# Kernel optimization log

Measured on AMD Instinct MI355X. Metric: run time of the kernel, lower is better.

Reference implementation:

```python
import jax, jax.numpy as jnp
import numpy as np

N_NODES = 100000
N_EDGES = 1600000
IN_CH = 128
OUT_CH = 128


def setup_inputs() -> dict:
    key = jax.random.key(0)
    k1, k2, k3 = jax.random.split(key, 3)
    x = jax.random.normal(k1, (N_NODES, IN_CH), dtype=jnp.float32)
    edge_index = jax.random.randint(k2, (2, N_EDGES), 0, N_NODES, dtype=jnp.int64)
    # glorot-like init for the linear weight, stored as [in, out]
    W = jax.random.normal(k3, (IN_CH, OUT_CH), dtype=jnp.float32) * (2.0 / (IN_CH + OUT_CH)) ** 0.5
    bias = jnp.zeros((OUT_CH,), dtype=jnp.float32)
    return {"x": x, "edge_index": edge_index, "W": W, "bias": bias}


def reference(x, edge_index, W, bias):
    N = x.shape[0]
    # linear transform (bias-free, matches Linear(in, out, bias=False))
    h = x @ W  # [N, out]

    # add self loops (improved=False -> fill_value = 1.0)
    loop = jnp.arange(N, dtype=edge_index.dtype)
    src = jnp.concatenate([edge_index[0], loop])
    dst = jnp.concatenate([edge_index[1], loop])
    ew = jnp.ones(src.shape[0], dtype=h.dtype)  # edge_weight None -> ones

    # symmetric GCN normalization: deg from dst, norm = d^-1/2[src] * w * d^-1/2[dst]
    deg = jax.ops.segment_sum(ew, dst, num_segments=N)
    deg_inv_sqrt = jnp.where(deg > 0, jax.lax.rsqrt(deg), 0.0)
    w = deg_inv_sqrt[src] * ew * deg_inv_sqrt[dst]

    # spmm aggregation: out[dst] += w * h[src]
    out = jax.ops.segment_sum(h[src] * w[:, None], dst, num_segments=N)
    return out + bias
```

## Files before the change

kernel.cpp:

```cpp
#include <hip/hip_runtime.h>
#include <hip/hip_bf16.h>

constexpr int kNodes = 100000;
constexpr int kEdges = 1600000;
constexpr int kCh    = 128;
constexpr int kCap   = 32;
constexpr int kLOvf  = 256;
constexpr int kBinShift = 7;
constexpr int kBinSize  = 1 << kBinShift;
constexpr int kBins  = (kNodes + kBinSize - 1) >> kBinShift;
constexpr int kABlocks = 128;
constexpr int kChunkCap = 32;
constexpr int kSpillCap = 64;
constexpr int kGemmBlocks = (kNodes + 127) / 128;

typedef __attribute__((ext_vector_type(8))) short short8;
typedef __attribute__((ext_vector_type(4))) float floatx4;
typedef __attribute__((ext_vector_type(4))) int   intx4;
typedef __attribute__((ext_vector_type(2))) float floatx2;


__global__ __launch_bounds__(512) void k_fused(const float* __restrict__ x,
                                               const float* __restrict__ W,
                                               const int* __restrict__ srcArr,
                                               const int* __restrict__ dstArr,
                                               unsigned* __restrict__ segs,
                                               int* __restrict__ segCnt,
                                               int* __restrict__ spillCnt,
                                               int* __restrict__ spillD,
                                               int* __restrict__ spillS,
                                               __hip_bfloat16* __restrict__ hs) {
  if (blockIdx.x < kABlocks) {
    __shared__ int lcnt[kBins];
    __shared__ int lspilln;
    for (int i = threadIdx.x; i < kBins; i += 512) lcnt[i] = 0;
    if (threadIdx.x == 0) lspilln = 0;
    __syncthreads();
    const intx4* d4 = (const intx4*)dstArr;
    const intx4* s4 = (const intx4*)srcArr;
    unsigned* myseg = segs + (long)blockIdx.x * kBins * kChunkCap;
    for (int i = blockIdx.x * 512 + (int)threadIdx.x; i < kEdges / 4; i += kABlocks * 512) {
      intx4 dv = __builtin_nontemporal_load(d4 + i);
      intx4 sv = __builtin_nontemporal_load(s4 + i);
      #pragma unroll
      for (int k = 0; k < 4; k++) {
        int d = dv[k], s = sv[k];
        int bin = d >> kBinShift;
        int pos = atomicAdd(&lcnt[bin], 1);
        if (pos < kChunkCap) {
          myseg[(bin << 5) + pos] = ((unsigned)(d & (kBinSize - 1)) << 17) | (unsigned)s;
        } else {
          int o = atomicAdd(&lspilln, 1);
          if (o < kSpillCap) {
            spillD[blockIdx.x * kSpillCap + o] = d;
            spillS[blockIdx.x * kSpillCap + o] = s;
          }
        }
      }
    }
    __syncthreads();
    for (int i = threadIdx.x; i < kBins; i += 512) {
      int c = lcnt[i];
      segCnt[blockIdx.x * kBins + i] = c < kChunkCap ? c : kChunkCap;
    }
    if (threadIdx.x == 0) {
      int n = lspilln;
      spillCnt[blockIdx.x] = n < kSpillCap ? n : kSpillCap;
    }
    return;
  }

  if (blockIdx.x == kABlocks && threadIdx.x < 64) {
    ((float*)(hs + (long)kNodes * kCh))[threadIdx.x] = 0.0f;
  }

  __shared__ short8 Bf[2048];
  for (int e = threadIdx.x; e < 2048; e += 512) {
    int lane = e & 63, c = (e >> 6) & 3, tt = e >> 8;
    int quad = lane >> 4, mcol = lane & 15;
    short8 v;
    #pragma unroll
    for (int j = 0; j < 8; j++) {
      __hip_bfloat16 h = __float2bfloat16(W[(c * 32 + quad * 8 + j) * kCh + tt * 16 + mcol]);
      v[j] = *(short*)&h;
    }
    Bf[e] = v;
  }
  __syncthreads();

  int wave = threadIdx.x >> 6;
  int lane = threadIdx.x & 63;
  int quad = lane >> 4;
  int mcol = lane & 15;
  int gb = blockIdx.x - kABlocks;
  long rowBase = ((long)gb * 8 + wave) * 16;
  if (rowBase >= kNodes) return;

  long arow = rowBase + mcol;
  if (arow >= kNodes) arow = kNodes - 1;
  const float* xp = x + arow * kCh;
  short8 afrag[4];
  #pragma unroll
  for (int c = 0; c < 4; c++) {
    const floatx4* p = (const floatx4*)(xp + c * 32 + quad * 8);
    floatx4 v0 = __builtin_nontemporal_load(p);
    floatx4 v1 = __builtin_nontemporal_load(p + 1);
    #pragma unroll
    for (int j = 0; j < 4; j++) {
      __hip_bfloat16 h0 = __float2bfloat16(v0[j]);
      __hip_bfloat16 h1 = __float2bfloat16(v1[j]);
      afrag[c][j]     = *(short*)&h0;
      afrag[c][j + 4] = *(short*)&h1;
    }
  }

  #pragma unroll
  for (int t = 0; t < 8; t++) {
    floatx4 acc = {0.f, 0.f, 0.f, 0.f};
    #pragma unroll
    for (int c = 0; c < 4; c++) {
      short8 b = Bf[(t * 4 + c) * 64 + lane];
      acc = __builtin_amdgcn_mfma_f32_16x16x32_bf16(afrag[c], b, acc, 0, 0, 0);
    }
    #pragma unroll
    for (int i = 0; i < 4; i++) {
      long r = rowBase + quad * 4 + i;
      if (r < kNodes) {
        __hip_bfloat16 h = __float2bfloat16(acc[i]);
        __builtin_nontemporal_store(*(short*)&h, (short*)hs + r * kCh + t * 16 + mcol);
      }
    }
  }
}


__global__ __launch_bounds__(256) void k_dinv(const unsigned* __restrict__ segs,
                                              const int* __restrict__ segCnt,
                                              const int* __restrict__ spillCnt,
                                              const int* __restrict__ spillD,
                                              float* __restrict__ dinv) {
  __shared__ int lsn[kABlocks];
  __shared__ int lsp[kABlocks];
  __shared__ int hist[kBinSize];
  int bin = blockIdx.x;
  for (int i = threadIdx.x; i < kABlocks; i += 256) {
    lsn[i] = segCnt[i * kBins + bin];
    lsp[i] = spillCnt[i];
  }
  for (int i = threadIdx.x; i < kBinSize; i += 256) hist[i] = 0;
  __syncthreads();

  for (int slot = threadIdx.x; slot < kABlocks * kChunkCap; slot += 256) {
    int blk = slot >> 5, pos = slot & 31;
    if (pos < lsn[blk]) {
      unsigned e = segs[((long)blk * kBins + bin) * kChunkCap + pos];
      atomicAdd(&hist[e >> 17], 1);
    }
  }
  for (int i = threadIdx.x; i < kABlocks * kSpillCap; i += 256) {
    int blk = i >> 6, o = i & 63;
    if (o < lsp[blk]) {
      int d = spillD[blk * kSpillCap + o];
      if ((d >> kBinShift) == bin) atomicAdd(&hist[d & (kBinSize - 1)], 1);
    }
  }
  __syncthreads();
  int base = bin << kBinShift;
  for (int i = threadIdx.x; i < kBinSize; i += 256) {
    int node = base + i;
    if (node < kNodes) dinv[node] = rsqrtf((float)(hist[i] + 1));
  }
  if (bin == 0 && threadIdx.x == 0) dinv[kNodes] = 0.0f;
}


__global__ __launch_bounds__(512) void k_agg(const unsigned* __restrict__ segs,
                                             const int* __restrict__ segCnt,
                                             const int* __restrict__ spillCnt,
                                             const int* __restrict__ spillD,
                                             const int* __restrict__ spillS,
                                             const float* __restrict__ dinv,
                                             const __hip_bfloat16* __restrict__ hs,
                                             const float* __restrict__ bias,
                                             float* __restrict__ out) {
  __shared__ int lsn[kABlocks];
  __shared__ int lsp[kABlocks];
  __shared__ int lcnt[kBinSize];
  __shared__ __align__(16) int lbkt[kBinSize][kCap];
  __shared__ unsigned lovf[kLOvf];
  __shared__ int lovfn;

  int bin  = blockIdx.x;
  int base = bin << kBinShift;

  for (int i = threadIdx.x; i < kABlocks; i += 512) {
    lsn[i] = segCnt[i * kBins + bin];
    lsp[i] = spillCnt[i];
  }
  for (int i = threadIdx.x; i < kBinSize; i += 512) lcnt[i] = 0;
  if (threadIdx.x == 0) lovfn = 0;
  __syncthreads();

  for (int slot = threadIdx.x; slot < kABlocks * kChunkCap; slot += 512) {
    int blk = slot >> 5, pos = slot & 31;
    if (pos < lsn[blk]) {
      unsigned e = segs[((long)blk * kBins + bin) * kChunkCap + pos];
      int r = (int)(e >> 17);
      int p = atomicAdd(&lcnt[r], 1);
      if (p < kCap) lbkt[r][p] = (int)(e & 0x1ffff);
      else { int o = atomicAdd(&lovfn, 1); if (o < kLOvf) lovf[o] = ((unsigned)r << 17) | (e & 0x1ffff); }
    }
  }
  for (int i = threadIdx.x; i < kABlocks * kSpillCap; i += 512) {
    int blk = i >> 6, o = i & 63;
    if (o < lsp[blk]) {
      int d = spillD[blk * kSpillCap + o];
      if ((d >> kBinShift) == bin) {
        int r = d & (kBinSize - 1);
        int s = spillS[blk * kSpillCap + o];
        int p = atomicAdd(&lcnt[r], 1);
        if (p < kCap) lbkt[r][p] = s;
        else { int o2 = atomicAdd(&lovfn, 1); if (o2 < kLOvf) lovf[o2] = ((unsigned)r << 17) | (unsigned)s; }
      }
    }
  }
  __syncthreads();

  for (int r = threadIdx.x; r < kBinSize; r += 512) {
    int c = lcnt[r]; if (c > kCap) c = kCap;
    int cP = (c + 7) & ~7; if (cP > kCap) cP = kCap;
    for (int p = c; p < cP; p++) lbkt[r][p] = kNodes;
  }
  __syncthreads();

  int wave = threadIdx.x >> 6;
  int lane = threadIdx.x & 63;
  const __hip_bfloat162* hbase = (const __hip_bfloat162*)hs;
  int novf = lovfn; if (novf > kLOvf) novf = kLOvf;
  float2 bsv = ((const float2*)bias)[lane];

  #define ISSUE(S, DV, V, B)                                                     \
    _Pragma("unroll")                                                            \
    for (int u = 0; u < 8; u++) S[u] = lbkt[r][(B) * 8 + u];                     \
    _Pragma("unroll")                                                            \
    for (int u = 0; u < 8; u++) { DV[u] = dinv[S[u]];                            \
      V[u] = hbase[(long)S[u] * (kCh / 2) + lane]; }

  #define CONSUME(DV, V)                                                         \
    _Pragma("unroll")                                                            \
    for (int u = 0; u < 8; u++) { float2 f = __bfloat1622float2(V[u]);           \
      acc0 = fmaf(DV[u], f.x, acc0); acc1 = fmaf(DV[u], f.y, acc1); }

  for (int t = 0; t < 16; t++) {
    int r = wave * 16 + t;
    int node = base + r;
    if (node >= kNodes) continue;

    float dd = dinv[node];
    float2 sf = __bfloat1622float2(hbase[(long)node * (kCh / 2) + lane]);
    float acc0 = dd * sf.x;
    float acc1 = dd * sf.y;

    int c = lcnt[r]; if (c > kCap) c = kCap;
    int nb = (c + 7) >> 3;

    if (nb > 0) {
      int sA[8], sB[8];
      float dvA[8], dvB[8];
      __hip_bfloat162 vA[8], vB[8];
      ISSUE(sA, dvA, vA, 0);
      for (int bb = 0; bb < nb; bb += 2) {
        if (bb + 1 < nb) { ISSUE(sB, dvB, vB, bb + 1); }
        CONSUME(dvA, vA);
        if (bb + 2 < nb) { ISSUE(sA, dvA, vA, bb + 2); }
        if (bb + 1 < nb) { CONSUME(dvB, vB); }
      }
    }

    for (int i = 0; i < novf; i++) {
      if ((int)(lovf[i] >> 17) == r) {
        int s = (int)(lovf[i] & 0x1ffff);
        float2 f = __bfloat1622float2(hbase[(long)s * (kCh / 2) + lane]);
        acc0 = fmaf(dinv[s], f.x, acc0);
        acc1 = fmaf(dinv[s], f.y, acc1);
      }
    }

    floatx2 o;
    o[0] = dd * acc0 + bsv.x;
    o[1] = dd * acc1 + bsv.y;
    __builtin_nontemporal_store(o, (floatx2*)(out + (long)node * kCh) + lane);
  }
  #undef ISSUE
  #undef CONSUME
}


extern "C" void kernel_launch(void* const* d_in, const int* in_sizes, int n_in,
                              void* d_out, int out_size, void* d_ws, size_t ws_size,
                              hipStream_t stream) {
  const float* x    = (const float*)d_in[0];
  const int*   ei   = (const int*)d_in[1];
  const float* W    = (const float*)d_in[2];
  const float* bias = (const float*)d_in[3];
  float* out = (float*)d_out;

  const int* srcArr = ei;
  const int* dstArr = ei + kEdges;

  char* ws = (char*)d_ws;
  size_t off = 0;
  __hip_bfloat16* hs = (__hip_bfloat16*)(ws + off);
  off += (size_t)(kNodes + 1) * kCh * 2;
  unsigned* segs = (unsigned*)(ws + off); off += (size_t)kABlocks * kBins * kChunkCap * 4;
  float* dinv    = (float*)   (ws + off); off += (size_t)(kNodes + 1) * 4;
  int*   segCnt  = (int*)     (ws + off); off += (size_t)kABlocks * kBins * 4;
  int*   spillCnt= (int*)     (ws + off); off += (size_t)kABlocks * 4;
  int*   spillD  = (int*)     (ws + off); off += (size_t)kABlocks * kSpillCap * 4;
  int*   spillS  = (int*)     (ws + off); off += (size_t)kABlocks * kSpillCap * 4;

  k_fused<<<kABlocks + kGemmBlocks, 512, 0, stream>>>(x, W, srcArr, dstArr,
                                                      segs, segCnt, spillCnt, spillD, spillS, hs);

  k_dinv<<<kBins, 256, 0, stream>>>(segs, segCnt, spillCnt, spillD, dinv);

  k_agg<<<kBins, 512, 0, stream>>>(segs, segCnt, spillCnt, spillD, spillS,
                                   dinv, hs, bias, out);
}
```

Before: 245.3 us.

## Gather four neighbor rows per wave with 16-byte loads and shuffle-reduce

Restructures the per-node gather so each wave splits into four 16-lane groups. Each group loads a different neighbor's full bf16 row with 128-bit loads instead of all 64 lanes reading one row with 32-bit loads. Partial sums are combined with cross-group shuffles, and padding drops from multiples of 8 to multiples of 4. The goal is fewer, wider memory instructions and more neighbor rows in flight, at the cost of eight accumulators, shuffle reduction and a select on output.

```diff
diff --git a/kernel.cpp b/kernel.cpp
--- a/kernel.cpp
+++ b/kernel.cpp
@@ -18,6 +18,14 @@
 typedef __attribute__((ext_vector_type(4))) float floatx4;
 typedef __attribute__((ext_vector_type(4))) int   intx4;
 typedef __attribute__((ext_vector_type(2))) float floatx2;
+
+__device__ __forceinline__ float2 bf2f(unsigned u) {
+  union { unsigned i; float f; } a, b;
+  a.i = u << 16;
+  b.i = u & 0xffff0000u;
+  float2 r; r.x = a.f; r.y = b.f;
+  return r;
+}
 
 
 __global__ __launch_bounds__(512) void k_fused(const float* __restrict__ x,
@@ -228,28 +236,18 @@
 
   for (int r = threadIdx.x; r < kBinSize; r += 512) {
     int c = lcnt[r]; if (c > kCap) c = kCap;
-    int cP = (c + 7) & ~7; if (cP > kCap) cP = kCap;
+    int cP = (c + 3) & ~3; if (cP > kCap) cP = kCap;
     for (int p = c; p < cP; p++) lbkt[r][p] = kNodes;
   }
   __syncthreads();
 
   int wave = threadIdx.x >> 6;
   int lane = threadIdx.x & 63;
-  const __hip_bfloat162* hbase = (const __hip_bfloat162*)hs;
+  int g    = lane >> 4;
+  int q    = lane & 15;
+  const short* hraw = (const short*)hs;
   int novf = lovfn; if (novf > kLOvf) novf = kLOvf;
-  float2 bsv = ((const float2*)bias)[lane];
-
-  #define ISSUE(S, DV, V, B)                                                     \
-    _Pragma("unroll")                                                            \
-    for (int u = 0; u < 8; u++) S[u] = lbkt[r][(B) * 8 + u];                     \
-    _Pragma("unroll")                                                            \
-    for (int u = 0; u < 8; u++) { DV[u] = dinv[S[u]];                            \
-      V[u] = hbase[(long)S[u] * (kCh / 2) + lane]; }
-
-  #define CONSUME(DV, V)                                                         \
-    _Pragma("unroll")                                                            \
-    for (int u = 0; u < 8; u++) { float2 f = __bfloat1622float2(V[u]);           \
-      acc0 = fmaf(DV[u], f.x, acc0); acc1 = fmaf(DV[u], f.y, acc1); }
+  float2 bsv = ((const float2*)bias)[q * 4 + g];
 
   for (int t = 0; t < 16; t++) {
     int r = wave * 16 + t;
@@ -257,42 +255,87 @@
     if (node >= kNodes) continue;
 
     float dd = dinv[node];
-    float2 sf = __bfloat1622float2(hbase[(long)node * (kCh / 2) + lane]);
-    float acc0 = dd * sf.x;
-    float acc1 = dd * sf.y;
+    float acc0, acc1, acc2, acc3, acc4, acc5, acc6, acc7;
+    {
+      intx4 sv = *(const intx4*)(hraw + (long)node * kCh + q * 8);
+      float w = (g == 0) ? dd : 0.0f;
+      float2 f0 = bf2f((unsigned)sv[0]);
+      float2 f1 = bf2f((unsigned)sv[1]);
+      float2 f2 = bf2f((unsigned)sv[2]);
+      float2 f3 = bf2f((unsigned)sv[3]);
+      acc0 = w * f0.x; acc1 = w * f0.y; acc2 = w * f1.x; acc3 = w * f1.y;
+      acc4 = w * f2.x; acc5 = w * f2.y; acc6 = w * f3.x; acc7 = w * f3.y;
+    }
 
     int c = lcnt[r]; if (c > kCap) c = kCap;
-    int nb = (c + 7) >> 3;
-
-    if (nb > 0) {
-      int sA[8], sB[8];
-      float dvA[8], dvB[8];
-      __hip_bfloat162 vA[8], vB[8];
-      ISSUE(sA, dvA, vA, 0);
-      for (int bb = 0; bb < nb; bb += 2) {
-        if (bb + 1 < nb) { ISSUE(sB, dvB, vB, bb + 1); }
-        CONSUME(dvA, vA);
-        if (bb + 2 < nb) { ISSUE(sA, dvA, vA, bb + 2); }
-        if (bb + 1 < nb) { CONSUME(dvB, vB); }
-      }
-    }
+    int nb = (c + 3) >> 2;
+
+    #define SLOT(V, D, B)                                                        \
+      intx4 V = {0, 0, 0, 0}; float D = 0.0f;                                    \
+      if ((B) < nb) {                                                            \
+        int sg = lbkt[r][(B) * 4 + g];                                           \
+        D = dinv[sg];                                                            \
+        V = *(const intx4*)(hraw + (long)sg * kCh + q * 8);                      \
+      }
+
+    #define EAT(V, D) {                                                          \
+      float2 f0 = bf2f((unsigned)V[0]);                                          \
+      float2 f1 = bf2f((unsigned)V[1]);                                          \
+      float2 f2 = bf2f((unsigned)V[2]);                                          \
+      float2 f3 = bf2f((unsigned)V[3]);                                          \
+      acc0 = fmaf(D, f0.x, acc0); acc1 = fmaf(D, f0.y, acc1);                    \
+      acc2 = fmaf(D, f1.x, acc2); acc3 = fmaf(D, f1.y, acc3);                    \
+      acc4 = fmaf(D, f2.x, acc4); acc5 = fmaf(D, f2.y, acc5);                    \
+      acc6 = fmaf(D, f3.x, acc6); acc7 = fmaf(D, f3.y, acc7); }
+
+    {
+      SLOT(v0, d0, 0) SLOT(v1, d1, 1) SLOT(v2, d2, 2) SLOT(v3, d3, 3)
+      EAT(v0, d0) EAT(v1, d1) EAT(v2, d2) EAT(v3, d3)
+    }
+    if (nb > 4) {
+      SLOT(v4, d4, 4) SLOT(v5, d5, 5) SLOT(v6, d6, 6) SLOT(v7, d7, 7)
+      EAT(v4, d4) EAT(v5, d5) EAT(v6, d6) EAT(v7, d7)
+    }
+    #undef SLOT
+    #undef EAT
+
+    acc0 += __shfl_xor(acc0, 16, 64); acc0 += __shfl_xor(acc0, 32, 64);
+    acc1 += __shfl_xor(acc1, 16, 64); acc1 += __shfl_xor(acc1, 32, 64);
+    acc2 += __shfl_xor(acc2, 16, 64); acc2 += __shfl_xor(acc2, 32, 64);
+    acc3 += __shfl_xor(acc3, 16, 64); acc3 += __shfl_xor(acc3, 32, 64);
+    acc4 += __shfl_xor(acc4, 16, 64); acc4 += __shfl_xor(acc4, 32, 64);
+    acc5 += __shfl_xor(acc5, 16, 64); acc5 += __shfl_xor(acc5, 32, 64);
+    acc6 += __shfl_xor(acc6, 16, 64); acc6 += __shfl_xor(acc6, 32, 64);
+    acc7 += __shfl_xor(acc7, 16, 64); acc7 += __shfl_xor(acc7, 32, 64);
 
     for (int i = 0; i < novf; i++) {
       if ((int)(lovf[i] >> 17) == r) {
         int s = (int)(lovf[i] & 0x1ffff);
-        float2 f = __bfloat1622float2(hbase[(long)s * (kCh / 2) + lane]);
-        acc0 = fmaf(dinv[s], f.x, acc0);
-        acc1 = fmaf(dinv[s], f.y, acc1);
-      }
-    }
-
+        float w = dinv[s];
+        intx4 v = *(const intx4*)(hraw + (long)s * kCh + q * 8);
+        float2 f0 = bf2f((unsigned)v[0]);
+        float2 f1 = bf2f((unsigned)v[1]);
+        float2 f2 = bf2f((unsigned)v[2]);
+        float2 f3 = bf2f((unsigned)v[3]);
+        acc0 = fmaf(w, f0.x, acc0); acc1 = fmaf(w, f0.y, acc1);
+        acc2 = fmaf(w, f1.x, acc2); acc3 = fmaf(w, f1.y, acc3);
+        acc4 = fmaf(w, f2.x, acc4); acc5 = fmaf(w, f2.y, acc5);
+        acc6 = fmaf(w, f3.x, acc6); acc7 = fmaf(w, f3.y, acc7);
+      }
+    }
+
+    float a0, a1;
+    switch (g) {
+      case 0: a0 = acc0; a1 = acc1; break;
+      case 1: a0 = acc2; a1 = acc3; break;
+      case 2: a0 = acc4; a1 = acc5; break;
+      default: a0 = acc6; a1 = acc7; break;
+    }
     floatx2 o;
-    o[0] = dd * acc0 + bsv.x;
-    o[1] = dd * acc1 + bsv.y;
-    __builtin_nontemporal_store(o, (floatx2*)(out + (long)node * kCh) + lane);
-  }
-  #undef ISSUE
-  #undef CONSUME
+    o[0] = dd * a0 + bsv.x;
+    o[1] = dd * a1 + bsv.y;
+    __builtin_nontemporal_store(o, (floatx2*)(out + (long)node * kCh) + q * 4 + g);
+  }
 }
 
 
```

New measurement: 235.6 us. -4.0%, faster.
